# Kernel optimization log

Measured on AMD Instinct MI355X. Metric: run time of the kernel, lower is better.

## Reference

```python
import jax, jax.numpy as jnp
import numpy as np

N_NODES = 100000
N_EDGES = 3200000
IN_F, HID, OUT = 3, 32, 1
NEG_SLOPE = 0.2


def _glorot(key, shape):
    fan_in, fan_out = shape[0], shape[-1]
    lim = jnp.sqrt(6.0 / (fan_in + fan_out)).astype(jnp.float32)
    return jax.random.uniform(key, shape, jnp.float32, -lim, lim)


def setup_inputs() -> dict:
    key = jax.random.key(0)
    ks = jax.random.split(key, 12)
    x = jax.random.normal(ks[0], (N_NODES, IN_F), jnp.float32)
    edge_index = jax.random.randint(ks[1], (2, N_EDGES), 0, N_NODES, jnp.int32)
    return {
        "x": x,
        "edge_index": edge_index,
        "W1": _glorot(ks[2], (IN_F, HID)),
        "att_src1": _glorot(ks[3], (1, HID))[0],
        "att_dst1": _glorot(ks[4], (1, HID))[0],
        "b1": jnp.zeros((HID,), jnp.float32),
        "W2": _glorot(ks[5], (HID, HID)),
        "att_src2": _glorot(ks[6], (1, HID))[0],
        "att_dst2": _glorot(ks[7], (1, HID))[0],
        "b2": jnp.zeros((HID,), jnp.float32),
        "Wl": _glorot(ks[8], (HID, OUT)),
        "bl": jnp.zeros((OUT,), jnp.float32),
    }


def gat_layer(x, src, dst, W, att_src, att_dst, b):
    # h: [N, HID] dense transform
    h = x @ W
    # per-node attention halves (compute once per node, gather per edge)
    a_s = h @ att_src  # [N]
    a_d = h @ att_dst  # [N]
    logits = jax.nn.leaky_relu(a_s[src] + a_d[dst], NEG_SLOPE)  # [E+N]
    # segment-softmax over incoming edges of each dst node
    m = jax.ops.segment_max(logits, dst, num_segments=N_NODES)
    m = jnp.where(jnp.isfinite(m), m, 0.0)
    ex = jnp.exp(logits - m[dst])
    denom = jax.ops.segment_sum(ex, dst, num_segments=N_NODES)
    coef = ex / (denom[dst] + 1e-16)
    # weighted scatter-aggregate of source messages
    out = jax.ops.segment_sum(coef[:, None] * h[src], dst, num_segments=N_NODES)
    return out + b


def reference(x, edge_index, W1, att_src1, att_dst1, b1, W2, att_src2, att_dst2, b2, Wl, bl):
    # PyG GATConv default: add self-loops
    loops = jnp.arange(N_NODES, dtype=edge_index.dtype)
    src = jnp.concatenate([edge_index[0], loops])
    dst = jnp.concatenate([edge_index[1], loops])
    h = gat_layer(x, src, dst, W1, att_src1, att_dst1, b1)
    h = jax.nn.relu(h)  # dropout is identity in eval
    h = gat_layer(h, src, dst, W2, att_src2, att_dst2, b2)
    h = jax.nn.relu(h)
    return h @ Wl + bl
```

## Files before the change

kernel.cpp:

```cpp
#include <hip/hip_runtime.h>
#include <hip/hip_fp16.h>

#define HID 32
#define BN 131
#define NBPAD 768
#define BSTRIDE 4608
#define CHUNK 4096

__device__ __forceinline__ float lrelu(float x) { return x > 0.0f ? x : 0.2f * x; }


struct BinSM {
    int stage[CHUNK];
    unsigned short sbid[CHUNK];
    int lhist[NBPAD], lexcl[NBPAD], lbase[NBPAD], lcur[NBPAD];
    int arr[256];
};
struct AggSM {
    int2  lpair[BSTRIDE];
    int   lhist[256], lscan[256], lcur[256];
    float adT[BN];
};
union FusedSM { BinSM bin; AggSM agg; };

template<int BLK>
__device__ __forceinline__ void binscatter_chunk(BinSM& S, int base,
        const int* __restrict__ src, const int* __restrict__ dst,
        int* __restrict__ cursor, unsigned int* __restrict__ packed,
        int NBr, int E)
{
    int t = threadIdx.x;
    for (int i = t; i < NBPAD; i += BLK) { S.lhist[i] = 0; S.lcur[i] = 0; }
    __syncthreads();
    int cnt = E - base; if (cnt > CHUNK) cnt = CHUNK;
    for (int i = t; i < cnt; i += BLK)
        atomicAdd(&S.lhist[dst[base + i] / BN], 1);
    __syncthreads();
    int b0 = 3 * t;
    int c0 = 0, c1 = 0, c2 = 0, s = 0;
    if (t < 256) {
        c0 = S.lhist[b0]; c1 = S.lhist[b0 + 1]; c2 = S.lhist[b0 + 2];
        s = c0 + c1 + c2;
        S.arr[t] = s;
    }
    __syncthreads();
    for (int o = 1; o < 256; o <<= 1) {
        int v = (t < 256 && t >= o) ? S.arr[t - o] : 0;
        __syncthreads();
        if (t < 256) S.arr[t] += v;
        __syncthreads();
    }
    if (t < 256) {
        int ex = S.arr[t] - s;
        int e0 = ex, e1 = ex + c0, e2 = ex + c0 + c1;
        S.lexcl[b0] = e0; S.lexcl[b0 + 1] = e1; S.lexcl[b0 + 2] = e2;
        for (int i = 0; i < c0; ++i) S.sbid[e0 + i] = (unsigned short)b0;
        for (int i = 0; i < c1; ++i) S.sbid[e1 + i] = (unsigned short)(b0 + 1);
        for (int i = 0; i < c2; ++i) S.sbid[e2 + i] = (unsigned short)(b0 + 2);
    }
    for (int b = t; b < NBr; b += BLK)
        if (S.lhist[b]) S.lbase[b] = b * BSTRIDE + atomicAdd(&cursor[b], S.lhist[b]);
    __syncthreads();
    for (int i = t; i < cnt; i += BLK) {
        int d = dst[base + i];
        int sv = src[base + i];
        int b = d / BN;
        int dl = d - b * BN;
        int idx = S.lexcl[b] + atomicAdd(&S.lcur[b], 1);
        S.stage[idx] = (int)((unsigned)sv | ((unsigned)dl << 17));
    }
    __syncthreads();
    for (int i = t; i < cnt; i += BLK) {
        int b = S.sbid[i];
        int gpos = S.lbase[b] + (i - S.lexcl[b]);
        if (gpos < (b + 1) * BSTRIDE)
            packed[gpos] = (unsigned)S.stage[i];
    }
}

template<int BLK>
__device__ __forceinline__ void build_csr_pair(int2* lpair, float* adT,
        int* lhist, int* lscan, int* lcur,
        const unsigned int* __restrict__ pk, int cnt,
        const float* __restrict__ a_s, const float* __restrict__ a_d,
        int nodeBase, int N)
{
    int t = threadIdx.x;
    if (t < 256) { lhist[t] = 0; lcur[t] = 0; }
    if (t < BN) { int n = nodeBase + t; adT[t] = (n < N) ? a_d[n] : 0.0f; }
    __syncthreads();
    for (int i = t; i < cnt; i += BLK)
        atomicAdd(&lhist[(pk[i] >> 17) & 255], 1);
    __syncthreads();
    if (t < 256) lscan[t] = lhist[t];
    __syncthreads();
    for (int o = 1; o < 256; o <<= 1) {
        int v = (t < 256 && t >= o) ? lscan[t - o] : 0;
        __syncthreads();
        if (t < 256) lscan[t] += v;
        __syncthreads();
    }
    for (int i = t; i < cnt; i += BLK) {
        unsigned p = pk[i];
        int dl = (p >> 17) & 255;
        int sv = (int)(p & 0x1FFFF);
        float e = __expf(lrelu(a_s[sv] + adT[dl]));
        int pos = atomicAdd(&lcur[dl], 1);
        lpair[(lscan[dl] - lhist[dl]) + pos] = make_int2((int)p, __float_as_int(e));
    }
    __syncthreads();
}

__device__ __forceinline__ void agg_node(const __half* __restrict__ hh,
                                         float ex_self, const float* __restrict__ b,
                                         int n, int f,
                                         const int2* lpair,
                                         int off, int dg, float& vx, float& vy)
{
    float den = ex_self;
    float2 hs = __half22float2(*(const __half2*)(hh + (size_t)n * HID + 2 * f));
    float accx = ex_self * hs.x;
    float accy = ex_self * hs.y;
    int j = 0;
    for (; j + 8 <= dg; j += 8) {
        int2 p0 = lpair[off + j + 0], p1 = lpair[off + j + 1];
        int2 p2 = lpair[off + j + 2], p3 = lpair[off + j + 3];
        int2 p4 = lpair[off + j + 4], p5 = lpair[off + j + 5];
        int2 p6 = lpair[off + j + 6], p7 = lpair[off + j + 7];
        int s0 = p0.x & 0x1FFFF, s1 = p1.x & 0x1FFFF;
        int s2 = p2.x & 0x1FFFF, s3 = p3.x & 0x1FFFF;
        int s4 = p4.x & 0x1FFFF, s5 = p5.x & 0x1FFFF;
        int s6 = p6.x & 0x1FFFF, s7 = p7.x & 0x1FFFF;
        __half2 h0 = *(const __half2*)(hh + (size_t)s0 * HID + 2 * f);
        __half2 h1 = *(const __half2*)(hh + (size_t)s1 * HID + 2 * f);
        __half2 h2 = *(const __half2*)(hh + (size_t)s2 * HID + 2 * f);
        __half2 h3 = *(const __half2*)(hh + (size_t)s3 * HID + 2 * f);
        __half2 h4 = *(const __half2*)(hh + (size_t)s4 * HID + 2 * f);
        __half2 h5 = *(const __half2*)(hh + (size_t)s5 * HID + 2 * f);
        __half2 h6 = *(const __half2*)(hh + (size_t)s6 * HID + 2 * f);
        __half2 h7 = *(const __half2*)(hh + (size_t)s7 * HID + 2 * f);
        float e0 = __int_as_float(p0.y), e1 = __int_as_float(p1.y);
        float e2 = __int_as_float(p2.y), e3 = __int_as_float(p3.y);
        float e4 = __int_as_float(p4.y), e5 = __int_as_float(p5.y);
        float e6 = __int_as_float(p6.y), e7 = __int_as_float(p7.y);
        float2 q0 = __half22float2(h0), q1 = __half22float2(h1);
        float2 q2 = __half22float2(h2), q3 = __half22float2(h3);
        float2 q4 = __half22float2(h4), q5 = __half22float2(h5);
        float2 q6 = __half22float2(h6), q7 = __half22float2(h7);
        den += ((e0 + e1) + (e2 + e3)) + ((e4 + e5) + (e6 + e7));
        accx = fmaf(e0, q0.x, accx); accy = fmaf(e0, q0.y, accy);
        accx = fmaf(e1, q1.x, accx); accy = fmaf(e1, q1.y, accy);
        accx = fmaf(e2, q2.x, accx); accy = fmaf(e2, q2.y, accy);
        accx = fmaf(e3, q3.x, accx); accy = fmaf(e3, q3.y, accy);
        accx = fmaf(e4, q4.x, accx); accy = fmaf(e4, q4.y, accy);
        accx = fmaf(e5, q5.x, accx); accy = fmaf(e5, q5.y, accy);
        accx = fmaf(e6, q6.x, accx); accy = fmaf(e6, q6.y, accy);
        accx = fmaf(e7, q7.x, accx); accy = fmaf(e7, q7.y, accy);
    }
    for (; j < dg; ++j) {
        int2 p0 = lpair[off + j];
        int s0 = p0.x & 0x1FFFF;
        float e0 = __int_as_float(p0.y);
        float2 q0 = __half22float2(*(const __half2*)(hh + (size_t)s0 * HID + 2 * f));
        den += e0;
        accx = fmaf(e0, q0.x, accx);
        accy = fmaf(e0, q0.y, accy);
    }
    float inv = 1.0f / (den + 1e-16f);
    vx = fmaxf(accx * inv + b[2 * f], 0.0f);
    vy = fmaxf(accy * inv + b[2 * f + 1], 0.0f);
}

__device__ __forceinline__ void epi_mid(int n, int f, float vx, float vy,
        const float* __restrict__ W2, const float* __restrict__ as2w,
        const float* __restrict__ ad2w,
        __half* __restrict__ hh_out, float* __restrict__ as_out,
        float* __restrict__ ad_out)
{
    float hx = 0.0f, hy = 0.0f;
    #pragma unroll
    for (int k = 0; k < 16; ++k) {
        float va = __shfl(vx, k, 16);
        float vb = __shfl(vy, k, 16);
        float2 w0 = *(const float2*)(W2 + (2 * k) * HID + 2 * f);
        float2 w1 = *(const float2*)(W2 + (2 * k + 1) * HID + 2 * f);
        hx = fmaf(va, w0.x, hx); hy = fmaf(va, w0.y, hy);
        hx = fmaf(vb, w1.x, hx); hy = fmaf(vb, w1.y, hy);
    }
    *(__half2*)(hh_out + (size_t)n * HID + 2 * f) = __floats2half2_rn(hx, hy);
    float as = hx * as2w[2 * f] + hy * as2w[2 * f + 1];
    float ad = hx * ad2w[2 * f] + hy * ad2w[2 * f + 1];
    #pragma unroll
    for (int m2 = 8; m2 >= 1; m2 >>= 1) {
        as += __shfl_xor(as, m2, 16);
        ad += __shfl_xor(ad, m2, 16);
    }
    if (f == 0) { as_out[n] = as; ad_out[n] = ad; }
}

__device__ __forceinline__ void grid_bar(int* bar, int target)
{
    __syncthreads();
    if (threadIdx.x == 0) {
        __threadfence();
        __hip_atomic_fetch_add(bar, 1, __ATOMIC_RELEASE, __HIP_MEMORY_SCOPE_AGENT);
        while (__hip_atomic_load(bar, __ATOMIC_ACQUIRE, __HIP_MEMORY_SCOPE_AGENT) < target)
            __builtin_amdgcn_s_sleep(8);
        __threadfence();
    }
    __syncthreads();
}

__global__ void k_zero_bar(int* __restrict__ bar)
{
    if (threadIdx.x < 4) bar[threadIdx.x] = 0;
}

__global__ void __launch_bounds__(512) k_fused(
    const float* __restrict__ x, const int* __restrict__ src, const int* __restrict__ dst,
    const float* __restrict__ W1, const float* __restrict__ as1w,
    const float* __restrict__ ad1w, const float* __restrict__ b1,
    const float* __restrict__ W2, const float* __restrict__ as2w,
    const float* __restrict__ ad2w, const float* __restrict__ b2,
    const float* __restrict__ Wl, const float* __restrict__ bl,
    __half* __restrict__ h1h, __half* __restrict__ h2h,
    unsigned int* __restrict__ packed,
    float* __restrict__ a_s1, float* __restrict__ a_d1,
    float* __restrict__ a_s2, float* __restrict__ a_d2,
    int* __restrict__ cursor, int* __restrict__ bar,
    float* __restrict__ out, int N, int E, int NBr)
{
    __shared__ FusedSM sm;
    int t = threadIdx.x, bk = blockIdx.x;
    int nth = gridDim.x * 512, gtid = bk * 512 + t;

    for (int i = gtid; i < NBPAD; i += nth) cursor[i] = 0;
    for (int idx = gtid; idx < N * HID; idx += nth) {
        int n = idx >> 5, f = idx & 31;
        float x0 = x[n * 3 + 0], x1 = x[n * 3 + 1], x2 = x[n * 3 + 2];
        float hv = x0 * W1[f] + x1 * W1[HID + f] + x2 * W1[2 * HID + f];
        h1h[(size_t)n * HID + f] = __float2half(hv);
        float as = hv * as1w[f];
        float ad = hv * ad1w[f];
        #pragma unroll
        for (int m = 16; m >= 1; m >>= 1) {
            as += __shfl_xor(as, m, 32);
            ad += __shfl_xor(ad, m, 32);
        }
        if (f == 0) { a_s1[n] = as; a_d1[n] = ad; }
    }
    grid_bar(bar, gridDim.x);

    int nch = (E + CHUNK - 1) / CHUNK;
    for (int c = bk; c < nch; c += gridDim.x) {
        binscatter_chunk<512>(sm.bin, c * CHUNK, src, dst, cursor, packed, NBr, E);
        __syncthreads();
    }
    grid_bar(bar, 2 * gridDim.x);

    int cnt = cursor[bk]; if (cnt > BSTRIDE) cnt = BSTRIDE;
    build_csr_pair<512>(sm.agg.lpair, sm.agg.adT,
                        sm.agg.lhist, sm.agg.lscan, sm.agg.lcur,
                        packed + (size_t)bk * BSTRIDE, cnt, a_s1, a_d1, bk * BN, N);
    {
        int g = t >> 4, f = t & 15;
        for (int dl = g; dl < BN; dl += 32) {
            int n = bk * BN + dl;
            if (n >= N) continue;
            int off = sm.agg.lscan[dl] - sm.agg.lhist[dl];
            int dg = sm.agg.lhist[dl];
            float exs = __expf(lrelu(a_s1[n] + sm.agg.adT[dl]));
            float vx, vy;
            agg_node(h1h, exs, b1, n, f, sm.agg.lpair, off, dg, vx, vy);
            epi_mid(n, f, vx, vy, W2, as2w, ad2w, h2h, a_s2, a_d2);
        }
    }
    grid_bar(bar, 3 * gridDim.x);

    if (t < BN) { int n = bk * BN + t; sm.agg.adT[t] = (n < N) ? a_d2[n] : 0.0f; }
    __syncthreads();
    for (int i = t; i < cnt; i += 512) {
        int pw = sm.agg.lpair[i].x;
        int sv = pw & 0x1FFFF;
        int dl = (pw >> 17) & 255;
        float e = __expf(lrelu(a_s2[sv] + sm.agg.adT[dl]));
        sm.agg.lpair[i] = make_int2(pw, __float_as_int(e));
    }
    __syncthreads();
    {
        int g = t >> 4, f = t & 15;
        for (int dl = g; dl < BN; dl += 32) {
            int n = bk * BN + dl;
            if (n >= N) continue;
            int off = sm.agg.lscan[dl] - sm.agg.lhist[dl];
            int dg = sm.agg.lhist[dl];
            float exs = __expf(lrelu(a_s2[n] + sm.agg.adT[dl]));
            float vx, vy;
            agg_node(h2h, exs, b2, n, f, sm.agg.lpair, off, dg, vx, vy);
            float y = vx * Wl[2 * f] + vy * Wl[2 * f + 1];
            #pragma unroll
            for (int m2 = 8; m2 >= 1; m2 >>= 1)
                y += __shfl_xor(y, m2, 16);
            if (f == 0) out[n] = y + bl[0];
        }
    }
}


__global__ void k_transform1(const float* __restrict__ x,
                             const float* __restrict__ W1,
                             const float* __restrict__ att_src,
                             const float* __restrict__ att_dst,
                             __half* __restrict__ hh,
                             float* __restrict__ a_s,
                             float* __restrict__ a_d,
                             int* __restrict__ cursor, int N)
{
    int tid = blockIdx.x * blockDim.x + threadIdx.x;
    if (tid < NBPAD) cursor[tid] = 0;
    int n = tid >> 5, f = tid & 31;
    if (n >= N) return;
    float x0 = x[n * 3 + 0], x1 = x[n * 3 + 1], x2 = x[n * 3 + 2];
    float hv = x0 * W1[f] + x1 * W1[HID + f] + x2 * W1[2 * HID + f];
    hh[(size_t)n * HID + f] = __float2half(hv);
    float as = hv * att_src[f];
    float ad = hv * att_dst[f];
    #pragma unroll
    for (int m = 16; m >= 1; m >>= 1) {
        as += __shfl_xor(as, m, 32);
        ad += __shfl_xor(ad, m, 32);
    }
    if (f == 0) { a_s[n] = as; a_d[n] = ad; }
}

__global__ void __launch_bounds__(256) k_binscatter(const int* __restrict__ src,
        const int* __restrict__ dst, int* __restrict__ cursor,
        unsigned int* __restrict__ packed, int NBr, int E)
{
    __shared__ BinSM S;
    binscatter_chunk<256>(S, blockIdx.x * CHUNK, src, dst, cursor, packed, NBr, E);
}

__global__ void __launch_bounds__(512) k_agg_mid_f(const __half* __restrict__ hh,
        const float* __restrict__ a_s, const float* __restrict__ a_d,
        const int* __restrict__ cursor, const unsigned int* __restrict__ packed,
        const float* __restrict__ b1, const float* __restrict__ W2,
        const float* __restrict__ as2w, const float* __restrict__ ad2w,
        __half* __restrict__ hh_out, float* __restrict__ as_out,
        float* __restrict__ ad_out, int N)
{
    __shared__ AggSM S;
    int bk = blockIdx.x, t = threadIdx.x;
    int cnt = cursor[bk]; if (cnt > BSTRIDE) cnt = BSTRIDE;
    build_csr_pair<512>(S.lpair, S.adT, S.lhist, S.lscan, S.lcur,
                        packed + (size_t)bk * BSTRIDE, cnt, a_s, a_d, bk * BN, N);
    int g = t >> 4, f = t & 15;
    for (int dl = g; dl < BN; dl += 32) {
        int n = bk * BN + dl;
        if (n >= N) continue;
        int off = S.lscan[dl] - S.lhist[dl];
        int dg = S.lhist[dl];
        float exs = __expf(lrelu(a_s[n] + S.adT[dl]));
        float vx, vy;
        agg_node(hh, exs, b1, n, f, S.lpair, off, dg, vx, vy);
        epi_mid(n, f, vx, vy, W2, as2w, ad2w, hh_out, as_out, ad_out);
    }
}

__global__ void __launch_bounds__(512) k_agg_out_f(const __half* __restrict__ hh,
        const float* __restrict__ a_s, const float* __restrict__ a_d,
        const int* __restrict__ cursor, const unsigned int* __restrict__ packed,
        const float* __restrict__ b2, const float* __restrict__ Wl,
        const float* __restrict__ bl, float* __restrict__ out, int N)
{
    __shared__ AggSM S;
    int bk = blockIdx.x, t = threadIdx.x;
    int cnt = cursor[bk]; if (cnt > BSTRIDE) cnt = BSTRIDE;
    build_csr_pair<512>(S.lpair, S.adT, S.lhist, S.lscan, S.lcur,
                        packed + (size_t)bk * BSTRIDE, cnt, a_s, a_d, bk * BN, N);
    int g = t >> 4, f = t & 15;
    for (int dl = g; dl < BN; dl += 32) {
        int n = bk * BN + dl;
        if (n >= N) continue;
        int off = S.lscan[dl] - S.lhist[dl];
        int dg = S.lhist[dl];
        float exs = __expf(lrelu(a_s[n] + S.adT[dl]));
        float vx, vy;
        agg_node(hh, exs, b2, n, f, S.lpair, off, dg, vx, vy);
        float y = vx * Wl[2 * f] + vy * Wl[2 * f + 1];
        #pragma unroll
        for (int m2 = 8; m2 >= 1; m2 >>= 1)
            y += __shfl_xor(y, m2, 16);
        if (f == 0) out[n] = y + bl[0];
    }
}

extern "C" void kernel_launch(void* const* d_in, const int* in_sizes, int n_in,
                              void* d_out, int out_size, void* d_ws, size_t ws_size,
                              hipStream_t stream)
{
    const float* x        = (const float*)d_in[0];
    const int*   eidx     = (const int*)d_in[1];
    const float* W1       = (const float*)d_in[2];
    const float* att_src1 = (const float*)d_in[3];
    const float* att_dst1 = (const float*)d_in[4];
    const float* b1       = (const float*)d_in[5];
    const float* W2       = (const float*)d_in[6];
    const float* att_src2 = (const float*)d_in[7];
    const float* att_dst2 = (const float*)d_in[8];
    const float* b2       = (const float*)d_in[9];
    const float* Wl       = (const float*)d_in[10];
    const float* bl       = (const float*)d_in[11];
    float* out = (float*)d_out;

    int N = in_sizes[0] / 3;
    int E = in_sizes[1] / 2;
    const int* src = eidx;
    const int* dst = eidx + E;
    int NBr = (N + BN - 1) / BN;

    size_t szNHh = (size_t)N * HID * 2;
    size_t szN4  = (size_t)N * 4;
    size_t szPK  = (size_t)NBr * BSTRIDE * 4;

    char* ws = (char*)d_ws;
    __half* h1h    = (__half*)ws; ws += szNHh;
    __half* h2h    = (__half*)ws; ws += szNHh;
    unsigned int* packed = (unsigned int*)ws; ws += szPK;
    float*  a_s1   = (float*)ws;  ws += szN4;
    float*  a_d1   = (float*)ws;  ws += szN4;
    float*  a_s2   = (float*)ws;  ws += szN4;
    float*  a_d2   = (float*)ws;  ws += szN4;
    int*    cursor = (int*)ws;    ws += NBPAD * 4;
    int*    bar    = (int*)ws;    ws += 64;

    int dev = 0, cus = 0, maxb = 0;
    hipGetDevice(&dev);
    hipDeviceGetAttribute(&cus, hipDeviceAttributeMultiprocessorCount, dev);
    hipOccupancyMaxActiveBlocksPerMultiprocessor(&maxb, k_fused, 512, 0);
    bool fused_ok = ((long)maxb * (long)cus >= (long)NBr) && (NBr <= NBPAD);

    if (fused_ok) {
        k_zero_bar<<<1, 64, 0, stream>>>(bar);
        k_fused<<<NBr, 512, 0, stream>>>(x, src, dst,
                                         W1, att_src1, att_dst1, b1,
                                         W2, att_src2, att_dst2, b2,
                                         Wl, bl, h1h, h2h, packed,
                                         a_s1, a_d1, a_s2, a_d2,
                                         cursor, bar, out, N, E, NBr);
    } else {
        const int B = 256;
        int gridNode32 = (N * HID + B - 1) / B;
        int gridBin    = (E + CHUNK - 1) / CHUNK;
        k_transform1<<<gridNode32, B, 0, stream>>>(x, W1, att_src1, att_dst1,
                                                   h1h, a_s1, a_d1, cursor, N);
        k_binscatter<<<gridBin, B, 0, stream>>>(src, dst, cursor, packed, NBr, E);
        k_agg_mid_f<<<NBr, 512, 0, stream>>>(h1h, a_s1, a_d1, cursor, packed,
                                             b1, W2, att_src2, att_dst2,
                                             h2h, a_s2, a_d2, N);
        k_agg_out_f<<<NBr, 512, 0, stream>>>(h2h, a_s2, a_d2, cursor, packed,
                                             b2, Wl, bl, out, N);
    }
}
```

Measured before the change: 249.7 us.

## Drop grid-barrier fused kernel in favor of separate kernel launches

```diff
diff --git a/kernel.cpp b/kernel.cpp
--- a/kernel.cpp
+++ b/kernel.cpp
@@ -21,7 +21,6 @@
     int   lhist[256], lscan[256], lcur[256];
     float adT[BN];
 };
-union FusedSM { BinSM bin; AggSM agg; };
 
 template<int BLK>
 __device__ __forceinline__ void binscatter_chunk(BinSM& S, int base,
@@ -198,114 +197,6 @@
     if (f == 0) { as_out[n] = as; ad_out[n] = ad; }
 }
 
-__device__ __forceinline__ void grid_bar(int* bar, int target)
-{
-    __syncthreads();
-    if (threadIdx.x == 0) {
-        __threadfence();
-        __hip_atomic_fetch_add(bar, 1, __ATOMIC_RELEASE, __HIP_MEMORY_SCOPE_AGENT);
-        while (__hip_atomic_load(bar, __ATOMIC_ACQUIRE, __HIP_MEMORY_SCOPE_AGENT) < target)
-            __builtin_amdgcn_s_sleep(8);
-        __threadfence();
-    }
-    __syncthreads();
-}
-
-__global__ void k_zero_bar(int* __restrict__ bar)
-{
-    if (threadIdx.x < 4) bar[threadIdx.x] = 0;
-}
-
-__global__ void __launch_bounds__(512) k_fused(
-    const float* __restrict__ x, const int* __restrict__ src, const int* __restrict__ dst,
-    const float* __restrict__ W1, const float* __restrict__ as1w,
-    const float* __restrict__ ad1w, const float* __restrict__ b1,
-    const float* __restrict__ W2, const float* __restrict__ as2w,
-    const float* __restrict__ ad2w, const float* __restrict__ b2,
-    const float* __restrict__ Wl, const float* __restrict__ bl,
-    __half* __restrict__ h1h, __half* __restrict__ h2h,
-    unsigned int* __restrict__ packed,
-    float* __restrict__ a_s1, float* __restrict__ a_d1,
-    float* __restrict__ a_s2, float* __restrict__ a_d2,
-    int* __restrict__ cursor, int* __restrict__ bar,
-    float* __restrict__ out, int N, int E, int NBr)
-{
-    __shared__ FusedSM sm;
-    int t = threadIdx.x, bk = blockIdx.x;
-    int nth = gridDim.x * 512, gtid = bk * 512 + t;
-
-    for (int i = gtid; i < NBPAD; i += nth) cursor[i] = 0;
-    for (int idx = gtid; idx < N * HID; idx += nth) {
-        int n = idx >> 5, f = idx & 31;
-        float x0 = x[n * 3 + 0], x1 = x[n * 3 + 1], x2 = x[n * 3 + 2];
-        float hv = x0 * W1[f] + x1 * W1[HID + f] + x2 * W1[2 * HID + f];
-        h1h[(size_t)n * HID + f] = __float2half(hv);
-        float as = hv * as1w[f];
-        float ad = hv * ad1w[f];
-        #pragma unroll
-        for (int m = 16; m >= 1; m >>= 1) {
-            as += __shfl_xor(as, m, 32);
-            ad += __shfl_xor(ad, m, 32);
-        }
-        if (f == 0) { a_s1[n] = as; a_d1[n] = ad; }
-    }
-    grid_bar(bar, gridDim.x);
-
-    int nch = (E + CHUNK - 1) / CHUNK;
-    for (int c = bk; c < nch; c += gridDim.x) {
-        binscatter_chunk<512>(sm.bin, c * CHUNK, src, dst, cursor, packed, NBr, E);
-        __syncthreads();
-    }
-    grid_bar(bar, 2 * gridDim.x);
-
-    int cnt = cursor[bk]; if (cnt > BSTRIDE) cnt = BSTRIDE;
-    build_csr_pair<512>(sm.agg.lpair, sm.agg.adT,
-                        sm.agg.lhist, sm.agg.lscan, sm.agg.lcur,
-                        packed + (size_t)bk * BSTRIDE, cnt, a_s1, a_d1, bk * BN, N);
-    {
-        int g = t >> 4, f = t & 15;
-        for (int dl = g; dl < BN; dl += 32) {
-            int n = bk * BN + dl;
-            if (n >= N) continue;
-            int off = sm.agg.lscan[dl] - sm.agg.lhist[dl];
-            int dg = sm.agg.lhist[dl];
-            float exs = __expf(lrelu(a_s1[n] + sm.agg.adT[dl]));
-            float vx, vy;
-            agg_node(h1h, exs, b1, n, f, sm.agg.lpair, off, dg, vx, vy);
-            epi_mid(n, f, vx, vy, W2, as2w, ad2w, h2h, a_s2, a_d2);
-        }
-    }
-    grid_bar(bar, 3 * gridDim.x);
-
-    if (t < BN) { int n = bk * BN + t; sm.agg.adT[t] = (n < N) ? a_d2[n] : 0.0f; }
-    __syncthreads();
-    for (int i = t; i < cnt; i += 512) {
-        int pw = sm.agg.lpair[i].x;
-        int sv = pw & 0x1FFFF;
-        int dl = (pw >> 17) & 255;
-        float e = __expf(lrelu(a_s2[sv] + sm.agg.adT[dl]));
-        sm.agg.lpair[i] = make_int2(pw, __float_as_int(e));
-    }
-    __syncthreads();
-    {
-        int g = t >> 4, f = t & 15;
-        for (int dl = g; dl < BN; dl += 32) {
-            int n = bk * BN + dl;
-            if (n >= N) continue;
-            int off = sm.agg.lscan[dl] - sm.agg.lhist[dl];
-            int dg = sm.agg.lhist[dl];
-            float exs = __expf(lrelu(a_s2[n] + sm.agg.adT[dl]));
-            float vx, vy;
-            agg_node(h2h, exs, b2, n, f, sm.agg.lpair, off, dg, vx, vy);
-            float y = vx * Wl[2 * f] + vy * Wl[2 * f + 1];
-            #pragma unroll
-            for (int m2 = 8; m2 >= 1; m2 >>= 1)
-                y += __shfl_xor(y, m2, 16);
-            if (f == 0) out[n] = y + bl[0];
-        }
-    }
-}
-
 
 __global__ void k_transform1(const float* __restrict__ x,
                              const float* __restrict__ W1,
@@ -333,12 +224,12 @@
     if (f == 0) { a_s[n] = as; a_d[n] = ad; }
 }
 
-__global__ void __launch_bounds__(256) k_binscatter(const int* __restrict__ src,
+__global__ void __launch_bounds__(512) k_binscatter(const int* __restrict__ src,
         const int* __restrict__ dst, int* __restrict__ cursor,
         unsigned int* __restrict__ packed, int NBr, int E)
 {
     __shared__ BinSM S;
-    binscatter_chunk<256>(S, blockIdx.x * CHUNK, src, dst, cursor, packed, NBr, E);
+    binscatter_chunk<512>(S, blockIdx.x * CHUNK, src, dst, cursor, packed, NBr, E);
 }
 
 __global__ void __launch_bounds__(512) k_agg_mid_f(const __half* __restrict__ hh,
@@ -432,33 +323,17 @@
     float*  a_s2   = (float*)ws;  ws += szN4;
     float*  a_d2   = (float*)ws;  ws += szN4;
     int*    cursor = (int*)ws;    ws += NBPAD * 4;
-    int*    bar    = (int*)ws;    ws += 64;
-
-    int dev = 0, cus = 0, maxb = 0;
-    hipGetDevice(&dev);
-    hipDeviceGetAttribute(&cus, hipDeviceAttributeMultiprocessorCount, dev);
-    hipOccupancyMaxActiveBlocksPerMultiprocessor(&maxb, k_fused, 512, 0);
-    bool fused_ok = ((long)maxb * (long)cus >= (long)NBr) && (NBr <= NBPAD);
-
-    if (fused_ok) {
-        k_zero_bar<<<1, 64, 0, stream>>>(bar);
-        k_fused<<<NBr, 512, 0, stream>>>(x, src, dst,
-                                         W1, att_src1, att_dst1, b1,
-                                         W2, att_src2, att_dst2, b2,
-                                         Wl, bl, h1h, h2h, packed,
-                                         a_s1, a_d1, a_s2, a_d2,
-                                         cursor, bar, out, N, E, NBr);
-    } else {
-        const int B = 256;
-        int gridNode32 = (N * HID + B - 1) / B;
-        int gridBin    = (E + CHUNK - 1) / CHUNK;
-        k_transform1<<<gridNode32, B, 0, stream>>>(x, W1, att_src1, att_dst1,
-                                                   h1h, a_s1, a_d1, cursor, N);
-        k_binscatter<<<gridBin, B, 0, stream>>>(src, dst, cursor, packed, NBr, E);
-        k_agg_mid_f<<<NBr, 512, 0, stream>>>(h1h, a_s1, a_d1, cursor, packed,
-                                             b1, W2, att_src2, att_dst2,
-                                             h2h, a_s2, a_d2, N);
-        k_agg_out_f<<<NBr, 512, 0, stream>>>(h2h, a_s2, a_d2, cursor, packed,
-                                             b2, Wl, bl, out, N);
-    }
-}
+
+    const int B = 256;
+    int gridNode32 = (N * HID + B - 1) / B;
+    int gridBin    = (E + CHUNK - 1) / CHUNK;
+
+    k_transform1<<<gridNode32, B, 0, stream>>>(x, W1, att_src1, att_dst1,
+                                               h1h, a_s1, a_d1, cursor, N);
+    k_binscatter<<<gridBin, 512, 0, stream>>>(src, dst, cursor, packed, NBr, E);
+    k_agg_mid_f<<<NBr, 512, 0, stream>>>(h1h, a_s1, a_d1, cursor, packed,
+                                         b1, W2, att_src2, att_dst2,
+                                         h2h, a_s2, a_d2, N);
+    k_agg_out_f<<<NBr, 512, 0, stream>>>(h2h, a_s2, a_d2, cursor, packed,
+                                         b2, Wl, bl, out, N);
+}
```

Measured after the change: 246.5 us. About the same (-1.3%).
